# Kernel tuning notes

Measured on AMD Instinct MI355X. Metric: run time of the kernel, lower is better.

The kernel has to match this reference:

```python
import jax, jax.numpy as jnp
import numpy as np

B, C_IN, C_OUT, H, W = 16, 256, 256, 64, 64
RANK, ORDER = 16, 2
EPS = 1e-5


def setup_inputs() -> dict:
    key = jax.random.key(0)
    k1, k2, k3 = jax.random.split(key, 3)
    x = jax.random.normal(k1, (B, C_IN, H, W), dtype=jnp.float32)
    # torch init: w_core ~ N(0, 1/(C_in*rank)), w_out ~ N(0, 1/rank)
    w_core = jax.random.normal(k2, (RANK, C_IN, RANK), dtype=jnp.float32) * (1.0 / (C_IN * RANK))
    w_out = jax.random.normal(k3, (RANK, C_OUT, RANK), dtype=jnp.float32) * (1.0 / RANK)
    return {"x": x, "w_core": w_core, "w_out": w_out}


def reference(x, w_core, w_out):
    # Per-pixel tensor-ring 1x1 conv.
    # Original chain for order=2 (share_core):
    #   T = einsum('achw,rck->arhwk', x, w_core)
    #   out = einsum('aebcf,afbcg,gdh->aedbch', T, T, w_out)
    #   y   = einsum('arohwr->aohw', out)   # ring trace over e==h
    # Equivalent: M[a,h,w] is rank x rank; P = M^order; y_d = tr(P @ W_d)
    M = jnp.einsum('achw,rck->ahwrk', x, w_core)  # [B,H,W,r,r]
    P = M
    for _ in range(ORDER - 1):
        P = jnp.einsum('ahwef,ahwfg->ahweg', P, M)
    y = jnp.einsum('ahweg,gde->adhw', P, w_out)  # [B,C_out,H,W]
    # InstanceNorm2d (affine=False, biased variance) + Softsign
    mean = jnp.mean(y, axis=(2, 3), keepdims=True)
    var = jnp.var(y, axis=(2, 3), keepdims=True)
    yn = (y - mean) * jax.lax.rsqrt(var + EPS)
    return yn / (1.0 + jnp.abs(yn))
```

## Files before the change

### kernel.cpp

```cpp
#include <hip/hip_runtime.h>

#define HW 4096
#define NC 256
#define ND 256

typedef _Float16 half4_t __attribute__((ext_vector_type(4)));
typedef _Float16 half8_t __attribute__((ext_vector_type(8)));
typedef float floatx4 __attribute__((ext_vector_type(4)));

#define MSCALE 64.0f
#define INV_MSCALE2 (1.0f / 4096.0f)

__global__ __launch_bounds__(256) void prep_weights(
        const float* __restrict__ w_core, const float* __restrict__ w_out,
        _Float16* __restrict__ W1p, _Float16* __restrict__ W2p) {
    int tid = blockIdx.x * 256 + threadIdx.x;
    int l   = tid & 63;
    int ks  = (tid >> 6) & 7;
    int rt  = (tid >> 9) & 15;
    int sel = tid >> 13;
    int row = l & 15, kg = l >> 4;
    half8_t v;
    if (sel == 0) {
        int rk = rt * 16 + row, r = rk >> 4, k = rk & 15;
#pragma unroll
        for (int j = 0; j < 8; ++j) {
            int c = ks * 32 + kg * 8 + j;
            v[j] = (_Float16)(w_core[r * 4096 + c * 16 + k] * MSCALE);
        }
        *(half8_t*)&W1p[(size_t)((rt * 8 + ks) * 64 + l) * 8] = v;
    } else {
        int d = rt * 16 + row;
#pragma unroll
        for (int j = 0; j < 8; ++j) {
            int eg = ks * 32 + kg * 8 + j, e = eg >> 4, g = eg & 15;
            v[j] = (_Float16)w_out[g * 4096 + d * 16 + e];
        }
        *(half8_t*)&W2p[(size_t)((rt * 8 + ks) * 64 + l) * 8] = v;
    }
}

__global__ __launch_bounds__(256, 2) void compute_y(
        const float* __restrict__ x, const _Float16* __restrict__ W1p,
        const _Float16* __restrict__ W2p, float* __restrict__ y) {
    __shared__ ushort MT[64 * 256];
    __shared__ ushort PL[64 * 256];

    const int t   = threadIdx.x;
    const int l   = t & 63;
    const int w   = t >> 6;
    const int a   = blockIdx.x >> 6;
    const int pixbase = (blockIdx.x & 63) * 64;
    const int row16 = l & 15;
    const int kg    = l >> 4;

    const int lpix = w * 16 + row16;
    const int wpix = pixbase + lpix;
    const float* xa = x + (size_t)a * NC * HW;

    half8_t bx[8];
#pragma unroll
    for (int ks = 0; ks < 8; ++ks) {
#pragma unroll
        for (int j = 0; j < 8; ++j) {
            int c = ks * 32 + kg * 8 + j;
            bx[ks][j] = (_Float16)xa[(size_t)c * HW + wpix];
        }
    }

    const half8_t* W1v = (const half8_t*)W1p;
    const int psw = lpix & 7;
#pragma unroll
    for (int rtg = 0; rtg < 4; ++rtg) {
        floatx4 acc[4] = {{0.f,0.f,0.f,0.f},{0.f,0.f,0.f,0.f},
                          {0.f,0.f,0.f,0.f},{0.f,0.f,0.f,0.f}};
#pragma unroll
        for (int ks = 0; ks < 8; ++ks) {
#pragma unroll
            for (int i = 0; i < 4; ++i) {
                int rt = rtg * 4 + i;
                acc[i] = __builtin_amdgcn_mfma_f32_16x16x32_f16(
                             W1v[(rt * 8 + ks) * 64 + l], bx[ks], acc[i], 0, 0, 0);
            }
        }
#pragma unroll
        for (int i = 0; i < 4; ++i) {
            int rt  = rtg * 4 + i;
            int rk4 = rt * 4 + kg;
            half4_t hv;
#pragma unroll
            for (int r2 = 0; r2 < 4; ++r2) hv[r2] = (_Float16)acc[i][r2];
            *(half4_t*)&MT[lpix * 256 + ((rk4 ^ psw) << 2)] = hv;
        }
    }
    __syncthreads();

    {
        const int p   = t >> 2;
        const int q   = t & 3;
        const int pswb = p & 7;
        float Af[4][16];
#pragma unroll
        for (int i = 0; i < 4; ++i) {
            int e = q * 4 + i;
#pragma unroll
            for (int f4 = 0; f4 < 4; ++f4) {
                half4_t v = *(const half4_t*)&MT[p * 256 + (((e * 4 + f4) ^ pswb) << 2)];
#pragma unroll
                for (int j = 0; j < 4; ++j) Af[i][f4 * 4 + j] = (float)v[j];
            }
        }
        float Pacc[4][16];
#pragma unroll
        for (int i = 0; i < 4; ++i)
#pragma unroll
            for (int g = 0; g < 16; ++g) Pacc[i][g] = 0.f;
#pragma unroll
        for (int f = 0; f < 16; ++f) {
            float Bg[16];
#pragma unroll
            for (int g4 = 0; g4 < 4; ++g4) {
                half4_t v = *(const half4_t*)&MT[p * 256 + (((f * 4 + g4) ^ pswb) << 2)];
#pragma unroll
                for (int j = 0; j < 4; ++j) Bg[g4 * 4 + j] = (float)v[j];
            }
#pragma unroll
            for (int i = 0; i < 4; ++i)
#pragma unroll
                for (int g = 0; g < 16; ++g)
                    Pacc[i][g] = fmaf(Af[i][f], Bg[g], Pacc[i][g]);
        }
#pragma unroll
        for (int i = 0; i < 4; ++i) {
            int e = q * 4 + i;
#pragma unroll
            for (int h = 0; h < 2; ++h) {
                half8_t hv;
#pragma unroll
                for (int j = 0; j < 8; ++j) hv[j] = (_Float16)Pacc[i][h * 8 + j];
                *(half8_t*)&PL[p * 256 + (((e * 2 + h) ^ pswb) << 3)] = hv;
            }
        }
    }
    __syncthreads();

    half8_t pb[8];
#pragma unroll
    for (int ks = 0; ks < 8; ++ks)
        pb[ks] = *(const half8_t*)&PL[lpix * 256 + (((ks * 4 + kg) ^ psw) << 3)];

    float* ya = y + (size_t)a * ND * HW + pixbase + lpix;
    const half8_t* W2v = (const half8_t*)W2p;
#pragma unroll
    for (int dtg = 0; dtg < 4; ++dtg) {
        floatx4 acc[4] = {{0.f,0.f,0.f,0.f},{0.f,0.f,0.f,0.f},
                          {0.f,0.f,0.f,0.f},{0.f,0.f,0.f,0.f}};
#pragma unroll
        for (int ks = 0; ks < 8; ++ks) {
#pragma unroll
            for (int i = 0; i < 4; ++i) {
                int dt = dtg * 4 + i;
                acc[i] = __builtin_amdgcn_mfma_f32_16x16x32_f16(
                             W2v[(dt * 8 + ks) * 64 + l], pb[ks], acc[i], 0, 0, 0);
            }
        }
#pragma unroll
        for (int i = 0; i < 4; ++i) {
            int d0 = (dtg * 4 + i) * 16 + kg * 4;
#pragma unroll
            for (int r2 = 0; r2 < 4; ++r2)
                ya[(size_t)(d0 + r2) * HW] = acc[i][r2] * INV_MSCALE2;
        }
    }
}

__global__ __launch_bounds__(256) void stats_kernel(
        const float* __restrict__ y, float* __restrict__ mean_o,
        float* __restrict__ istd_o) {
    const int ad = blockIdx.x;
    const float* row = y + (size_t)ad * HW;
    const int t = threadIdx.x;
    float s = 0.f, ss = 0.f;
#pragma unroll
    for (int q = 0; q < 4; ++q) {
        float4 v = *(const float4*)&row[4 * (t + q * 256)];
        s  += v.x + v.y + v.z + v.w;
        ss += v.x * v.x + v.y * v.y + v.z * v.z + v.w * v.w;
    }
#pragma unroll
    for (int off = 32; off > 0; off >>= 1) {
        s  += __shfl_down(s, off);
        ss += __shfl_down(ss, off);
    }
    __shared__ float ps[4], pq[4];
    if ((t & 63) == 0) { ps[t >> 6] = s; pq[t >> 6] = ss; }
    __syncthreads();
    if (t == 0) {
        s  = ps[0] + ps[1] + ps[2] + ps[3];
        ss = pq[0] + pq[1] + pq[2] + pq[3];
        float mean = s * (1.f / HW);
        float var  = ss * (1.f / HW) - mean * mean;
        mean_o[ad] = mean;
        istd_o[ad] = rsqrtf(var + 1e-5f);
    }
}

__global__ __launch_bounds__(256) void finalize_kernel(
        float* __restrict__ y, const float* __restrict__ mean_a,
        const float* __restrict__ istd_a) {
    const int i4 = blockIdx.x * 256 + threadIdx.x;
    const int ad = i4 >> 10;
    const float m = mean_a[ad], s = istd_a[ad];
    float4 v = ((const float4*)y)[i4];
    float vv[4] = {v.x, v.y, v.z, v.w};
#pragma unroll
    for (int lq = 0; lq < 4; ++lq) {
        float z = (vv[lq] - m) * s;
        vv[lq] = z / (1.f + fabsf(z));
    }
    ((float4*)y)[i4] = make_float4(vv[0], vv[1], vv[2], vv[3]);
}

extern "C" void kernel_launch(void* const* d_in, const int* in_sizes, int n_in,
                              void* d_out, int out_size, void* d_ws, size_t ws_size,
                              hipStream_t stream) {
    const float* x      = (const float*)d_in[0];
    const float* w_core = (const float*)d_in[1];
    const float* w_out  = (const float*)d_in[2];
    float* y = (float*)d_out;

    _Float16* W1p = (_Float16*)d_ws;
    _Float16* W2p = W1p + 65536;
    float* mean_a = (float*)(W2p + 65536);
    float* istd_a = mean_a + 4096;

    prep_weights<<<64, 256, 0, stream>>>(w_core, w_out, W1p, W2p);
    compute_y<<<1024, 256, 0, stream>>>(x, W1p, W2p, y);
    stats_kernel<<<4096, 256, 0, stream>>>(y, mean_a, istd_a);
    finalize_kernel<<<16384, 256, 0, stream>>>(y, mean_a, istd_a);
}
```

Baseline: 94.39 us.

## Fuse instance-norm statistics into compute kernel and stage weights through LDS

Moves the per-channel sum and sum-of-squares reduction into the main compute kernel using atomics, which removes the separate stats pass that re-read all of y. Output is transposed through shared memory so the y stores are coalesced. Weight tiles are staged into double-buffered LDS instead of being read per-lane from global memory. The 16x16 matrix square now uses packed float2 FMAs. In exchange the kernel keeps 16 accumulators live and adds extra barriers and atomics, which may raise register pressure.

```diff
diff --git a/kernel.cpp b/kernel.cpp
--- a/kernel.cpp
+++ b/kernel.cpp
@@ -6,6 +6,7 @@
 
 typedef _Float16 half4_t __attribute__((ext_vector_type(4)));
 typedef _Float16 half8_t __attribute__((ext_vector_type(8)));
+typedef float floatx2 __attribute__((ext_vector_type(2)));
 typedef float floatx4 __attribute__((ext_vector_type(4)));
 
 #define MSCALE 64.0f
@@ -16,19 +17,19 @@
         _Float16* __restrict__ W1p, _Float16* __restrict__ W2p) {
     int tid = blockIdx.x * 256 + threadIdx.x;
     int l   = tid & 63;
-    int ks  = (tid >> 6) & 7;
-    int rt  = (tid >> 9) & 15;
+    int rt  = (tid >> 6) & 15;
+    int ks  = (tid >> 10) & 7;
     int sel = tid >> 13;
     int row = l & 15, kg = l >> 4;
     half8_t v;
     if (sel == 0) {
-        int rk = rt * 16 + row, r = rk >> 4, k = rk & 15;
+        int r = rt, k = row;
 #pragma unroll
         for (int j = 0; j < 8; ++j) {
             int c = ks * 32 + kg * 8 + j;
             v[j] = (_Float16)(w_core[r * 4096 + c * 16 + k] * MSCALE);
         }
-        *(half8_t*)&W1p[(size_t)((rt * 8 + ks) * 64 + l) * 8] = v;
+        *(half8_t*)&W1p[(size_t)((ks * 16 + rt) * 64 + l) * 8] = v;
     } else {
         int d = rt * 16 + row;
 #pragma unroll
@@ -36,109 +37,122 @@
             int eg = ks * 32 + kg * 8 + j, e = eg >> 4, g = eg & 15;
             v[j] = (_Float16)w_out[g * 4096 + d * 16 + e];
         }
-        *(half8_t*)&W2p[(size_t)((rt * 8 + ks) * 64 + l) * 8] = v;
+        *(half8_t*)&W2p[(size_t)((ks * 16 + rt) * 64 + l) * 8] = v;
     }
 }
 
 __global__ __launch_bounds__(256, 2) void compute_y(
         const float* __restrict__ x, const _Float16* __restrict__ W1p,
-        const _Float16* __restrict__ W2p, float* __restrict__ y) {
-    __shared__ ushort MT[64 * 256];
-    __shared__ ushort PL[64 * 256];
-
-    const int t   = threadIdx.x;
-    const int l   = t & 63;
-    const int w   = t >> 6;
-    const int a   = blockIdx.x >> 6;
+        const _Float16* __restrict__ W2p, float* __restrict__ y,
+        float* __restrict__ ssum, float* __restrict__ ssq) {
+    __shared__ ushort R1[16384];
+    __shared__ ushort R2[16384];
+
+    const int t = threadIdx.x;
+    const int l = t & 63, w = t >> 6;
+    const int a = blockIdx.x >> 6;
     const int pixbase = (blockIdx.x & 63) * 64;
-    const int row16 = l & 15;
-    const int kg    = l >> 4;
-
+    const int row16 = l & 15, kg = l >> 4;
     const int lpix = w * 16 + row16;
     const int wpix = pixbase + lpix;
+    const int psw  = lpix & 7;
     const float* xa = x + (size_t)a * NC * HW;
 
     half8_t bx[8];
 #pragma unroll
-    for (int ks = 0; ks < 8; ++ks) {
-#pragma unroll
-        for (int j = 0; j < 8; ++j) {
-            int c = ks * 32 + kg * 8 + j;
-            bx[ks][j] = (_Float16)xa[(size_t)c * HW + wpix];
-        }
-    }
-
-    const half8_t* W1v = (const half8_t*)W1p;
-    const int psw = lpix & 7;
-#pragma unroll
-    for (int rtg = 0; rtg < 4; ++rtg) {
-        floatx4 acc[4] = {{0.f,0.f,0.f,0.f},{0.f,0.f,0.f,0.f},
-                          {0.f,0.f,0.f,0.f},{0.f,0.f,0.f,0.f}};
-#pragma unroll
+    for (int ks = 0; ks < 8; ++ks)
+#pragma unroll
+        for (int j = 0; j < 8; ++j)
+            bx[ks][j] = (_Float16)xa[(size_t)(ks * 32 + kg * 8 + j) * HW + wpix];
+
+    {
+        const float4* W1v4 = (const float4*)W1p;
+        float4* wbuf = (float4*)R2;
+        float4 st[4];
+#pragma unroll
+        for (int q = 0; q < 4; ++q) st[q] = W1v4[q * 256 + t];
+#pragma unroll
+        for (int q = 0; q < 4; ++q) wbuf[q * 256 + t] = st[q];
+
+        floatx4 acc[16];
+#pragma unroll
+        for (int i = 0; i < 16; ++i) acc[i] = (floatx4){0.f, 0.f, 0.f, 0.f};
+
         for (int ks = 0; ks < 8; ++ks) {
-#pragma unroll
-            for (int i = 0; i < 4; ++i) {
-                int rt = rtg * 4 + i;
-                acc[i] = __builtin_amdgcn_mfma_f32_16x16x32_f16(
-                             W1v[(rt * 8 + ks) * 64 + l], bx[ks], acc[i], 0, 0, 0);
-            }
-        }
-#pragma unroll
-        for (int i = 0; i < 4; ++i) {
-            int rt  = rtg * 4 + i;
+            if (ks < 7) {
+#pragma unroll
+                for (int q = 0; q < 4; ++q)
+                    st[q] = W1v4[(ks + 1) * 1024 + q * 256 + t];
+            }
+            __syncthreads();
+            const half8_t* af = (const half8_t*)R2 + (ks & 1) * 1024;
+#pragma unroll
+            for (int rt = 0; rt < 16; ++rt)
+                acc[rt] = __builtin_amdgcn_mfma_f32_16x16x32_f16(
+                              af[rt * 64 + l], bx[ks], acc[rt], 0, 0, 0);
+            if (ks < 7) {
+#pragma unroll
+                for (int q = 0; q < 4; ++q)
+                    wbuf[((ks + 1) & 1) * 1024 + q * 256 + t] = st[q];
+            }
+        }
+#pragma unroll
+        for (int rt = 0; rt < 16; ++rt) {
             int rk4 = rt * 4 + kg;
             half4_t hv;
 #pragma unroll
-            for (int r2 = 0; r2 < 4; ++r2) hv[r2] = (_Float16)acc[i][r2];
-            *(half4_t*)&MT[lpix * 256 + ((rk4 ^ psw) << 2)] = hv;
+            for (int r2 = 0; r2 < 4; ++r2) hv[r2] = (_Float16)acc[rt][r2];
+            *(half4_t*)&R1[lpix * 256 + ((rk4 ^ psw) << 2)] = hv;
         }
     }
     __syncthreads();
 
     {
-        const int p   = t >> 2;
-        const int q   = t & 3;
-        const int pswb = p & 7;
+        const int p = t >> 2, qe = t & 3, pswb = p & 7;
         float Af[4][16];
 #pragma unroll
         for (int i = 0; i < 4; ++i) {
-            int e = q * 4 + i;
+            int e = qe * 4 + i;
 #pragma unroll
             for (int f4 = 0; f4 < 4; ++f4) {
-                half4_t v = *(const half4_t*)&MT[p * 256 + (((e * 4 + f4) ^ pswb) << 2)];
+                half4_t v = *(const half4_t*)&R1[p * 256 + (((e * 4 + f4) ^ pswb) << 2)];
 #pragma unroll
                 for (int j = 0; j < 4; ++j) Af[i][f4 * 4 + j] = (float)v[j];
             }
         }
-        float Pacc[4][16];
+        floatx2 Pacc[4][8];
 #pragma unroll
         for (int i = 0; i < 4; ++i)
 #pragma unroll
-            for (int g = 0; g < 16; ++g) Pacc[i][g] = 0.f;
+            for (int g2 = 0; g2 < 8; ++g2) Pacc[i][g2] = (floatx2){0.f, 0.f};
 #pragma unroll
         for (int f = 0; f < 16; ++f) {
-            float Bg[16];
+            floatx2 Bg[8];
 #pragma unroll
             for (int g4 = 0; g4 < 4; ++g4) {
-                half4_t v = *(const half4_t*)&MT[p * 256 + (((f * 4 + g4) ^ pswb) << 2)];
-#pragma unroll
-                for (int j = 0; j < 4; ++j) Bg[g4 * 4 + j] = (float)v[j];
-            }
-#pragma unroll
-            for (int i = 0; i < 4; ++i)
-#pragma unroll
-                for (int g = 0; g < 16; ++g)
-                    Pacc[i][g] = fmaf(Af[i][f], Bg[g], Pacc[i][g]);
-        }
+                half4_t v = *(const half4_t*)&R1[p * 256 + (((f * 4 + g4) ^ pswb) << 2)];
+                Bg[g4 * 2]     = (floatx2){(float)v[0], (float)v[1]};
+                Bg[g4 * 2 + 1] = (floatx2){(float)v[2], (float)v[3]};
+            }
+#pragma unroll
+            for (int i = 0; i < 4; ++i) {
+                floatx2 a2 = {Af[i][f], Af[i][f]};
+#pragma unroll
+                for (int g2 = 0; g2 < 8; ++g2)
+                    Pacc[i][g2] = __builtin_elementwise_fma(a2, Bg[g2], Pacc[i][g2]);
+            }
+        }
+        __syncthreads();
 #pragma unroll
         for (int i = 0; i < 4; ++i) {
-            int e = q * 4 + i;
-#pragma unroll
-            for (int h = 0; h < 2; ++h) {
+            int e = qe * 4 + i;
+#pragma unroll
+            for (int h2 = 0; h2 < 2; ++h2) {
                 half8_t hv;
 #pragma unroll
-                for (int j = 0; j < 8; ++j) hv[j] = (_Float16)Pacc[i][h * 8 + j];
-                *(half8_t*)&PL[p * 256 + (((e * 2 + h) ^ pswb) << 3)] = hv;
+                for (int j = 0; j < 8; ++j)
+                    hv[j] = (_Float16)Pacc[i][h2 * 4 + (j >> 1)][j & 1];
+                *(half8_t*)&R2[p * 256 + (((e * 2 + h2) ^ pswb) << 3)] = hv;
             }
         }
     }
@@ -147,62 +161,85 @@
     half8_t pb[8];
 #pragma unroll
     for (int ks = 0; ks < 8; ++ks)
-        pb[ks] = *(const half8_t*)&PL[lpix * 256 + (((ks * 4 + kg) ^ psw) << 3)];
-
-    float* ya = y + (size_t)a * ND * HW + pixbase + lpix;
-    const half8_t* W2v = (const half8_t*)W2p;
-#pragma unroll
-    for (int dtg = 0; dtg < 4; ++dtg) {
-        floatx4 acc[4] = {{0.f,0.f,0.f,0.f},{0.f,0.f,0.f,0.f},
-                          {0.f,0.f,0.f,0.f},{0.f,0.f,0.f,0.f}};
-#pragma unroll
+        pb[ks] = *(const half8_t*)&R2[lpix * 256 + (((ks * 4 + kg) ^ psw) << 3)];
+
+    floatx4 cacc[16];
+#pragma unroll
+    for (int i = 0; i < 16; ++i) cacc[i] = (floatx4){0.f, 0.f, 0.f, 0.f};
+    {
+        const float4* W2v4 = (const float4*)W2p;
+        float4* wbuf = (float4*)R1;
+        float4 st[4];
+#pragma unroll
+        for (int q = 0; q < 4; ++q) st[q] = W2v4[q * 256 + t];
+        __syncthreads();
+#pragma unroll
+        for (int q = 0; q < 4; ++q) wbuf[q * 256 + t] = st[q];
+
         for (int ks = 0; ks < 8; ++ks) {
-#pragma unroll
-            for (int i = 0; i < 4; ++i) {
-                int dt = dtg * 4 + i;
-                acc[i] = __builtin_amdgcn_mfma_f32_16x16x32_f16(
-                             W2v[(dt * 8 + ks) * 64 + l], pb[ks], acc[i], 0, 0, 0);
-            }
-        }
-#pragma unroll
-        for (int i = 0; i < 4; ++i) {
-            int d0 = (dtg * 4 + i) * 16 + kg * 4;
-#pragma unroll
-            for (int r2 = 0; r2 < 4; ++r2)
-                ya[(size_t)(d0 + r2) * HW] = acc[i][r2] * INV_MSCALE2;
-        }
-    }
-}
-
-__global__ __launch_bounds__(256) void stats_kernel(
-        const float* __restrict__ y, float* __restrict__ mean_o,
-        float* __restrict__ istd_o) {
-    const int ad = blockIdx.x;
-    const float* row = y + (size_t)ad * HW;
-    const int t = threadIdx.x;
-    float s = 0.f, ss = 0.f;
-#pragma unroll
-    for (int q = 0; q < 4; ++q) {
-        float4 v = *(const float4*)&row[4 * (t + q * 256)];
-        s  += v.x + v.y + v.z + v.w;
-        ss += v.x * v.x + v.y * v.y + v.z * v.z + v.w * v.w;
-    }
-#pragma unroll
-    for (int off = 32; off > 0; off >>= 1) {
-        s  += __shfl_down(s, off);
-        ss += __shfl_down(ss, off);
-    }
-    __shared__ float ps[4], pq[4];
-    if ((t & 63) == 0) { ps[t >> 6] = s; pq[t >> 6] = ss; }
-    __syncthreads();
-    if (t == 0) {
-        s  = ps[0] + ps[1] + ps[2] + ps[3];
-        ss = pq[0] + pq[1] + pq[2] + pq[3];
-        float mean = s * (1.f / HW);
-        float var  = ss * (1.f / HW) - mean * mean;
-        mean_o[ad] = mean;
-        istd_o[ad] = rsqrtf(var + 1e-5f);
-    }
+            if (ks < 7) {
+#pragma unroll
+                for (int q = 0; q < 4; ++q)
+                    st[q] = W2v4[(ks + 1) * 1024 + q * 256 + t];
+            }
+            __syncthreads();
+            const half8_t* af = (const half8_t*)R1 + (ks & 1) * 1024;
+#pragma unroll
+            for (int dt = 0; dt < 16; ++dt)
+                cacc[dt] = __builtin_amdgcn_mfma_f32_16x16x32_f16(
+                               af[dt * 64 + l], pb[ks], cacc[dt], 0, 0, 0);
+            if (ks < 7) {
+#pragma unroll
+                for (int q = 0; q < 4; ++q)
+                    wbuf[((ks + 1) & 1) * 1024 + q * 256 + t] = st[q];
+            }
+        }
+    }
+
+    float* Yt = (float*)R2;
+    for (int h = 0; h < 2; ++h) {
+        __syncthreads();
+#pragma unroll
+        for (int dt = h * 8; dt < h * 8 + 8; ++dt) {
+            int ddb = (dt - h * 8) * 16 + kg * 4;
+#pragma unroll
+            for (int r2 = 0; r2 < 4; ++r2) {
+                int dd = ddb + r2;
+                Yt[dd * 64 + ((((lpix >> 2) ^ dd) & 15) << 2) + (lpix & 3)] =
+                    cacc[dt][r2] * INV_MSCALE2;
+            }
+        }
+        __syncthreads();
+        const int dd = t >> 1, half = t & 1;
+        float s = 0.f, sq = 0.f;
+        float* grow = y + (size_t)a * ND * HW + (size_t)(h * 128 + dd) * HW
+                        + pixbase + half * 32;
+#pragma unroll
+        for (int q = 0; q < 8; ++q) {
+            int group = half * 8 + q;
+            float4 v = *(float4*)&Yt[dd * 64 + (((group ^ dd) & 15) << 2)];
+            *(float4*)&grow[q * 4] = v;
+            s  += v.x + v.y + v.z + v.w;
+            sq += v.x * v.x + v.y * v.y + v.z * v.z + v.w * v.w;
+        }
+        s  += __shfl_xor(s, 1);
+        sq += __shfl_xor(sq, 1);
+        if (half == 0) {
+            int ad = a * 256 + h * 128 + dd;
+            atomicAdd(&ssum[ad], s);
+            atomicAdd(&ssq[ad], sq);
+        }
+    }
+}
+
+__global__ __launch_bounds__(256) void stats_finalize(
+        const float* __restrict__ ssum, const float* __restrict__ ssq,
+        float* __restrict__ mean_o, float* __restrict__ istd_o) {
+    int i = blockIdx.x * 256 + threadIdx.x;
+    float m = ssum[i] * (1.f / HW);
+    float v = ssq[i] * (1.f / HW) - m * m;
+    mean_o[i] = m;
+    istd_o[i] = rsqrtf(v + 1e-5f);
 }
 
 __global__ __launch_bounds__(256) void finalize_kernel(
@@ -231,11 +268,14 @@
 
     _Float16* W1p = (_Float16*)d_ws;
     _Float16* W2p = W1p + 65536;
-    float* mean_a = (float*)(W2p + 65536);
+    float* ssum   = (float*)(W2p + 65536);
+    float* ssq    = ssum + 4096;
+    float* mean_a = ssq + 4096;
     float* istd_a = mean_a + 4096;
 
+    hipMemsetAsync(ssum, 0, 2 * 4096 * sizeof(float), stream);
     prep_weights<<<64, 256, 0, stream>>>(w_core, w_out, W1p, W2p);
-    compute_y<<<1024, 256, 0, stream>>>(x, W1p, W2p, y);
-    stats_kernel<<<4096, 256, 0, stream>>>(y, mean_a, istd_a);
+    compute_y<<<1024, 256, 0, stream>>>(x, W1p, W2p, y, ssum, ssq);
+    stats_finalize<<<16, 256, 0, stream>>>(ssum, ssq, mean_a, istd_a);
     finalize_kernel<<<16384, 256, 0, stream>>>(y, mean_a, istd_a);
 }
```

Result: slower. 127.2 us (+34.7%).
